# Kernel optimization log

Hardware: AMD Instinct MI355X
Metric: run time of the kernel (lower is better)

The kernel has to match this reference:

```python
import jax, jax.numpy as jnp
import numpy as np

N_NODES = 100000


def gcn_conv(x, edge_index, W, b):
    # PyG GCNConv: add self-loops, symmetric normalization D^-1/2 (A+I) D^-1/2,
    # linear transform then scatter-add aggregation at target nodes, plus bias.
    n = x.shape[0]
    loops = jnp.arange(n, dtype=edge_index.dtype)
    src = jnp.concatenate([edge_index[0], loops])
    dst = jnp.concatenate([edge_index[1], loops])
    deg = jax.ops.segment_sum(jnp.ones_like(dst, dtype=x.dtype), dst, num_segments=n)
    dinv = jnp.where(deg > 0, jax.lax.rsqrt(deg), 0.0)
    norm = dinv[src] * dinv[dst]  # [E+N]
    h = x @ W                      # transform first (small out dim)
    msg = h[src] * norm[:, None]   # per-edge gather + scale
    out = jax.ops.segment_sum(msg, dst, num_segments=n)
    return out + b


def setup_inputs() -> dict:
    key = jax.random.key(0)
    k1, k2, k3, k4 = jax.random.split(key, 4)
    N, E = N_NODES, 3200000
    x = jax.random.normal(k1, (N, 132), dtype=jnp.float32)
    edge_index = jax.random.randint(k2, (2, E), 0, N, dtype=jnp.int64)
    W1 = jax.random.normal(k3, (132, 16), dtype=jnp.float32) * 0.1
    b1 = jnp.zeros((16,), dtype=jnp.float32)
    W2 = jax.random.normal(k4, (16, 10), dtype=jnp.float32) * 0.25
    b2 = jnp.zeros((10,), dtype=jnp.float32)
    return {"x": x, "edge_index": edge_index, "W1": W1, "b1": b1, "W2": W2, "b2": b2}


def reference(x, edge_index, W1, b1, W2, b2):
    h = gcn_conv(x, edge_index, W1, b1)
    h = jax.nn.relu(h)
    # F.dropout(training=self.training) is identity in eval mode
    h = gcn_conv(h, edge_index, W2, b2)
    return jax.nn.log_softmax(h, axis=1)
```

## Files before the change

kernel.cpp:

```cpp
#include <hip/hip_runtime.h>
#include <math.h>


#define F_IN 132
#define F1   16
#define F2   10
#define BSH  7
#define BSPAN 128
#define NB   782
#define CAP  4608
#define SPB  12500
#define SPLIT_BLOCKS 256

__device__ __forceinline__ unsigned short f2bf(float f) {
    unsigned u = __float_as_uint(f);
    u += 0x7FFFu + ((u >> 16) & 1u);
    return (unsigned short)(u >> 16);
}
__device__ __forceinline__ float bflo(unsigned u) { return __uint_as_float(u << 16); }
__device__ __forceinline__ float bfhi(unsigned u) { return __uint_as_float(u & 0xFFFF0000u); }

__global__ __launch_bounds__(1024) void k_split(const int* __restrict__ src,
                                                const int* __restrict__ dst,
                                                int* __restrict__ gcur,
                                                unsigned* __restrict__ entries, int E) {
    __shared__ unsigned le[SPB];
    __shared__ int h0[1024];
    __shared__ int h1[1024];
    __shared__ int off[NB];
    const int t = threadIdx.x;
    const int lo = blockIdx.x * SPB;
    const int hi = min(E, lo + SPB);
    const int n4 = (hi - lo) >> 2;
    h0[t] = 0;
    __syncthreads();
    const int4* d4 = (const int4*)(dst + lo);
    const int4* s4 = (const int4*)(src + lo);
    for (int i = t; i < n4; i += 1024) {
        int4 d = d4[i];
        atomicAdd(&h0[d.x >> BSH], 1);
        atomicAdd(&h0[d.y >> BSH], 1);
        atomicAdd(&h0[d.z >> BSH], 1);
        atomicAdd(&h0[d.w >> BSH], 1);
    }
    __syncthreads();
    int c = h0[t];
    h1[t] = c;
    __syncthreads();
    for (int o = 1; o < 1024; o <<= 1) {
        int v = (t >= o) ? h1[t - o] : 0;
        __syncthreads();
        h1[t] += v;
        __syncthreads();
    }
    int excl = h1[t] - c;
    if (t < NB) {
        int g = t * CAP + (c ? atomicAdd(&gcur[t], c) : 0);
        off[t] = g - excl;
    }
    h0[t] = excl;
    __syncthreads();
    for (int i = t; i < n4; i += 1024) {
        int4 d = d4[i];
        int4 s = s4[i];
        int p;
        p = atomicAdd(&h0[d.x >> BSH], 1); le[p] = ((unsigned)(d.x & 127) << 17) | (unsigned)s.x;
        p = atomicAdd(&h0[d.y >> BSH], 1); le[p] = ((unsigned)(d.y & 127) << 17) | (unsigned)s.y;
        p = atomicAdd(&h0[d.z >> BSH], 1); le[p] = ((unsigned)(d.z & 127) << 17) | (unsigned)s.z;
        p = atomicAdd(&h0[d.w >> BSH], 1); le[p] = ((unsigned)(d.w & 127) << 17) | (unsigned)s.w;
    }
    __syncthreads();
    for (int bk = t; bk < NB; bk += 1024) {
        int s0 = bk ? h1[bk - 1] : 0;
        int e0 = h1[bk];
        unsigned* gp = entries + off[bk] + s0;
        for (int i = s0; i < e0; ++i) *gp++ = le[i];
    }
}

__global__ void k_sortB(const int* __restrict__ gcur, unsigned* __restrict__ entries,
                        int* __restrict__ rps, int* __restrict__ rpe,
                        float* __restrict__ dinv, int N) {
    __shared__ unsigned le[CAP];
    __shared__ int hist[BSPAN];
    __shared__ int scn[BSPAN];
    __shared__ int cur[BSPAN];
    const int b = blockIdx.x;
    const int t = threadIdx.x;
    const int cbase = b * CAP;
    const int cnt = gcur[b];
    if (t < BSPAN) hist[t] = 0;
    __syncthreads();
    for (int i = t; i < cnt; i += 256) {
        unsigned p = entries[cbase + i];
        le[i] = p;
        atomicAdd(&hist[p >> 17], 1);
    }
    __syncthreads();
    if (t < BSPAN) scn[t] = hist[t];
    __syncthreads();
    #pragma unroll
    for (int o = 1; o < BSPAN; o <<= 1) {
        int v = (t < BSPAN && t >= o) ? scn[t - o] : 0;
        __syncthreads();
        if (t < BSPAN) scn[t] += v;
        __syncthreads();
    }
    if (t < BSPAN) {
        const int node = b * BSPAN + t;
        const int begl = scn[t] - hist[t];
        cur[t] = cbase + begl;
        if (node < N) {
            rps[node] = cbase + begl;
            rpe[node] = cbase + begl + hist[t];
            dinv[node] = rsqrtf((float)hist[t] + 1.0f);
        }
    }
    __syncthreads();
    for (int i = t; i < cnt; i += 256) {
        unsigned p = le[i];
        int pos = atomicAdd(&cur[p >> 17], 1);
        entries[pos] = p & 0x1FFFFu;
    }
}

__global__ void k_xw1(const float* __restrict__ x, const float* __restrict__ W1,
                      const float* __restrict__ dinv, unsigned short* __restrict__ g1u, int N) {
    __shared__ float xs[16 * F_IN];
    __shared__ float wsm[F_IN * F1];
    const int t = threadIdx.x;
    const int base = blockIdx.x * 16;
    for (int idx = t; idx < 528; idx += 256)
        ((float4*)wsm)[idx] = ((const float4*)W1)[idx];
    int nrows = N - base; if (nrows > 16) nrows = 16;
    const float4* xp4 = (const float4*)(x + (size_t)base * F_IN);
    const int span4 = nrows * 33;
    for (int idx = t; idx < span4; idx += 256) ((float4*)xs)[idx] = xp4[idx];
    __syncthreads();
    const int r = t >> 4;
    const int c = t & 15;
    if (r < nrows) {
        float acc = 0.f;
        #pragma unroll 4
        for (int k = 0; k < F_IN; ++k) acc += xs[r * F_IN + k] * wsm[k * F1 + c];
        g1u[(size_t)(base + r) * 16 + c] = f2bf(acc * dinv[base + r]);
    }
}

#define ACCU8(q, B) \
    acc[(B)+0] += bflo((q).x); acc[(B)+1] += bfhi((q).x); \
    acc[(B)+2] += bflo((q).y); acc[(B)+3] += bfhi((q).y); \
    acc[(B)+4] += bflo((q).z); acc[(B)+5] += bfhi((q).z); \
    acc[(B)+6] += bflo((q).w); acc[(B)+7] += bfhi((q).w);

__global__ void k_agg1(const int* __restrict__ rps, const int* __restrict__ rpe,
                       const unsigned* __restrict__ ssrc, const unsigned short* __restrict__ g1u,
                       const float* __restrict__ dinv, const float* __restrict__ b1,
                       const float* __restrict__ W2, unsigned short* __restrict__ g2u, int N) {
    __shared__ float w2s[F1 * F2];
    __shared__ float b1s[F1];
    if (threadIdx.x < F1 * F2) w2s[threadIdx.x] = W2[threadIdx.x];
    if (threadIdx.x < F1) b1s[threadIdx.x] = b1[threadIdx.x];
    __syncthreads();
    const int d = blockIdx.x * blockDim.x + threadIdx.x;
    if (d >= N) return;
    const int beg = rps[d], end = rpe[d];
    float acc[F1];
    #pragma unroll
    for (int j = 0; j < F1; ++j) acc[j] = 0.f;
    int e = beg;
    for (; e + 1 < end; e += 2) {
        int s0 = (int)ssrc[e];
        int s1 = (int)ssrc[e + 1];
        const uint4* r0 = (const uint4*)(g1u + (size_t)s0 * 16);
        const uint4* r1 = (const uint4*)(g1u + (size_t)s1 * 16);
        uint4 a0 = r0[0], a1 = r0[1];
        uint4 c0 = r1[0], c1 = r1[1];
        ACCU8(a0, 0) ACCU8(a1, 8)
        ACCU8(c0, 0) ACCU8(c1, 8)
    }
    if (e < end) {
        int s = (int)ssrc[e];
        const uint4* r = (const uint4*)(g1u + (size_t)s * 16);
        uint4 a0 = r[0], a1 = r[1];
        ACCU8(a0, 0) ACCU8(a1, 8)
    }
    {
        const uint4* r = (const uint4*)(g1u + (size_t)d * 16);
        uint4 a0 = r[0], a1 = r[1];
        ACCU8(a0, 0) ACCU8(a1, 8)
    }
    const float dv = dinv[d];
    float tt[F1];
    #pragma unroll
    for (int j = 0; j < F1; ++j) {
        float v = dv * acc[j] + b1s[j];
        tt[j] = v > 0.f ? v : 0.f;
    }
    float o[F2];
    #pragma unroll
    for (int c = 0; c < F2; ++c) {
        float a = 0.f;
        #pragma unroll
        for (int j = 0; j < F1; ++j) a += tt[j] * w2s[j * F2 + c];
        o[c] = dv * a;
    }
    unsigned w0 = ((unsigned)f2bf(o[1]) << 16) | f2bf(o[0]);
    unsigned w1 = ((unsigned)f2bf(o[3]) << 16) | f2bf(o[2]);
    unsigned w2 = ((unsigned)f2bf(o[5]) << 16) | f2bf(o[4]);
    unsigned w3 = ((unsigned)f2bf(o[7]) << 16) | f2bf(o[6]);
    unsigned w4 = ((unsigned)f2bf(o[9]) << 16) | f2bf(o[8]);
    uint4* op = (uint4*)(g2u + (size_t)d * 16);
    op[0] = make_uint4(w0, w1, w2, w3);
    op[1] = make_uint4(w4, 0u, 0u, 0u);
}

__global__ void k_agg2(const int* __restrict__ rps, const int* __restrict__ rpe,
                       const unsigned* __restrict__ ssrc, const unsigned short* __restrict__ g2u,
                       const float* __restrict__ dinv, const float* __restrict__ b2,
                       float* __restrict__ out, int N) {
    __shared__ float b2s[F2];
    if (threadIdx.x < F2) b2s[threadIdx.x] = b2[threadIdx.x];
    __syncthreads();
    const int d = blockIdx.x * blockDim.x + threadIdx.x;
    if (d >= N) return;
    const int beg = rps[d], end = rpe[d];
    float acc[F2];
    #pragma unroll
    for (int c = 0; c < F2; ++c) acc[c] = 0.f;
    int e = beg;
    for (; e + 1 < end; e += 2) {
        int s0 = (int)ssrc[e];
        int s1 = (int)ssrc[e + 1];
        const unsigned short* p0 = g2u + (size_t)s0 * 16;
        const unsigned short* p1 = g2u + (size_t)s1 * 16;
        uint4 a0 = *(const uint4*)(p0);
        unsigned a4 = *(const unsigned*)(p0 + 8);
        uint4 c0 = *(const uint4*)(p1);
        unsigned c4 = *(const unsigned*)(p1 + 8);
        ACCU8(a0, 0)
        acc[8] += bflo(a4); acc[9] += bfhi(a4);
        ACCU8(c0, 0)
        acc[8] += bflo(c4); acc[9] += bfhi(c4);
    }
    if (e < end) {
        int s = (int)ssrc[e];
        const unsigned short* p = g2u + (size_t)s * 16;
        uint4 a0 = *(const uint4*)(p);
        unsigned a4 = *(const unsigned*)(p + 8);
        ACCU8(a0, 0)
        acc[8] += bflo(a4); acc[9] += bfhi(a4);
    }
    {
        const unsigned short* p = g2u + (size_t)d * 16;
        uint4 a0 = *(const uint4*)(p);
        unsigned a4 = *(const unsigned*)(p + 8);
        ACCU8(a0, 0)
        acc[8] += bflo(a4); acc[9] += bfhi(a4);
    }
    const float dv = dinv[d];
    float v[F2];
    float m = -INFINITY;
    #pragma unroll
    for (int c = 0; c < F2; ++c) {
        v[c] = dv * acc[c] + b2s[c];
        m = fmaxf(m, v[c]);
    }
    float ssum = 0.f;
    #pragma unroll
    for (int c = 0; c < F2; ++c) ssum += expf(v[c] - m);
    float ls = logf(ssum);
    float* op = out + (size_t)d * F2;
    #pragma unroll
    for (int c = 0; c < F2; ++c) op[c] = v[c] - m - ls;
}

extern "C" void kernel_launch(void* const* d_in, const int* in_sizes, int n_in,
                              void* d_out, int out_size, void* d_ws, size_t ws_size,
                              hipStream_t stream) {
    const float* x  = (const float*)d_in[0];
    const int*   ei = (const int*)  d_in[1];
    const float* W1 = (const float*)d_in[2];
    const float* b1 = (const float*)d_in[3];
    const float* W2 = (const float*)d_in[4];
    const float* b2 = (const float*)d_in[5];
    float* out = (float*)d_out;

    const int N = in_sizes[0] / F_IN;
    const int E = in_sizes[1] / 2;
    const int* src = ei;
    const int* dst = ei + E;

    char* w = (char*)d_ws;
    int*            gcur    = (int*)w;            w += ((size_t)NB * 4 + 255) & ~255ull;
    int*            rps     = (int*)w;            w += ((size_t)N * 4 + 255) & ~255ull;
    int*            rpe     = (int*)w;            w += ((size_t)N * 4 + 255) & ~255ull;
    float*          dinv    = (float*)w;          w += ((size_t)N * 4 + 255) & ~255ull;
    unsigned short* g1u     = (unsigned short*)w; w += ((size_t)N * 16 * 2 + 255) & ~255ull;
    unsigned short* g2u     = (unsigned short*)w; w += ((size_t)N * 16 * 2 + 255) & ~255ull;
    unsigned*       entries = (unsigned*)w;

    hipMemsetAsync(gcur, 0, (size_t)NB * 4, stream);
    k_split<<<SPLIT_BLOCKS, 1024, 0, stream>>>(src, dst, gcur, entries, E);
    k_sortB<<<NB, 256, 0, stream>>>(gcur, entries, rps, rpe, dinv, N);
    k_xw1  <<<(N + 15) / 16, 256, 0, stream>>>(x, W1, dinv, g1u, N);
    k_agg1 <<<(N + 255) / 256, 256, 0, stream>>>(rps, rpe, entries, g1u, dinv, b1, W2, g2u, N);
    k_agg2 <<<(N + 255) / 256, 256, 0, stream>>>(rps, rpe, entries, g2u, dinv, b2, out, N);
}
```

Measured before the change: 169.3 us.

## Split each node's edge aggregation across four lanes with shuffle reduction

Both aggregation kernels now assign four threads per destination node, each walking a strided quarter of the node's edge list, then combine partial sums with xor shuffles before lane 0 finishes the epilogue. This raises parallelism and memory-level concurrency for the gather-heavy loops, since about 32 edges per node were previously serialized in one thread. The output write in the second layer is vectorized as well. It costs four times the threads and shuffle overhead, and three of every four lanes sit idle during the epilogue.

```diff
diff --git a/kernel.cpp b/kernel.cpp
--- a/kernel.cpp
+++ b/kernel.cpp
@@ -147,11 +147,11 @@
     }
 }
 
-#define ACCU8(q, B) \
-    acc[(B)+0] += bflo((q).x); acc[(B)+1] += bfhi((q).x); \
-    acc[(B)+2] += bflo((q).y); acc[(B)+3] += bfhi((q).y); \
-    acc[(B)+4] += bflo((q).z); acc[(B)+5] += bfhi((q).z); \
-    acc[(B)+6] += bflo((q).w); acc[(B)+7] += bfhi((q).w);
+#define ACCU8(qv, B) \
+    acc[(B)+0] += bflo((qv).x); acc[(B)+1] += bfhi((qv).x); \
+    acc[(B)+2] += bflo((qv).y); acc[(B)+3] += bfhi((qv).y); \
+    acc[(B)+4] += bflo((qv).z); acc[(B)+5] += bfhi((qv).z); \
+    acc[(B)+6] += bflo((qv).w); acc[(B)+7] += bfhi((qv).w);
 
 __global__ void k_agg1(const int* __restrict__ rps, const int* __restrict__ rpe,
                        const unsigned* __restrict__ ssrc, const unsigned short* __restrict__ g1u,
@@ -162,57 +162,54 @@
     if (threadIdx.x < F1 * F2) w2s[threadIdx.x] = W2[threadIdx.x];
     if (threadIdx.x < F1) b1s[threadIdx.x] = b1[threadIdx.x];
     __syncthreads();
-    const int d = blockIdx.x * blockDim.x + threadIdx.x;
+    const int gid = blockIdx.x * blockDim.x + threadIdx.x;
+    const int d = gid >> 2;
+    const int q = gid & 3;
     if (d >= N) return;
     const int beg = rps[d], end = rpe[d];
     float acc[F1];
     #pragma unroll
     for (int j = 0; j < F1; ++j) acc[j] = 0.f;
-    int e = beg;
-    for (; e + 1 < end; e += 2) {
-        int s0 = (int)ssrc[e];
-        int s1 = (int)ssrc[e + 1];
-        const uint4* r0 = (const uint4*)(g1u + (size_t)s0 * 16);
-        const uint4* r1 = (const uint4*)(g1u + (size_t)s1 * 16);
-        uint4 a0 = r0[0], a1 = r0[1];
-        uint4 c0 = r1[0], c1 = r1[1];
-        ACCU8(a0, 0) ACCU8(a1, 8)
-        ACCU8(c0, 0) ACCU8(c1, 8)
-    }
-    if (e < end) {
+    for (int e = beg + q; e < end; e += 4) {
         int s = (int)ssrc[e];
         const uint4* r = (const uint4*)(g1u + (size_t)s * 16);
         uint4 a0 = r[0], a1 = r[1];
         ACCU8(a0, 0) ACCU8(a1, 8)
     }
-    {
+    if (q == 0) {
         const uint4* r = (const uint4*)(g1u + (size_t)d * 16);
         uint4 a0 = r[0], a1 = r[1];
         ACCU8(a0, 0) ACCU8(a1, 8)
     }
-    const float dv = dinv[d];
-    float tt[F1];
-    #pragma unroll
-    for (int j = 0; j < F1; ++j) {
-        float v = dv * acc[j] + b1s[j];
-        tt[j] = v > 0.f ? v : 0.f;
-    }
-    float o[F2];
-    #pragma unroll
-    for (int c = 0; c < F2; ++c) {
-        float a = 0.f;
+    #pragma unroll
+    for (int j = 0; j < F1; ++j) acc[j] += __shfl_xor(acc[j], 1);
+    #pragma unroll
+    for (int j = 0; j < F1; ++j) acc[j] += __shfl_xor(acc[j], 2);
+    if (q == 0) {
+        const float dv = dinv[d];
+        float tt[F1];
         #pragma unroll
-        for (int j = 0; j < F1; ++j) a += tt[j] * w2s[j * F2 + c];
-        o[c] = dv * a;
-    }
-    unsigned w0 = ((unsigned)f2bf(o[1]) << 16) | f2bf(o[0]);
-    unsigned w1 = ((unsigned)f2bf(o[3]) << 16) | f2bf(o[2]);
-    unsigned w2 = ((unsigned)f2bf(o[5]) << 16) | f2bf(o[4]);
-    unsigned w3 = ((unsigned)f2bf(o[7]) << 16) | f2bf(o[6]);
-    unsigned w4 = ((unsigned)f2bf(o[9]) << 16) | f2bf(o[8]);
-    uint4* op = (uint4*)(g2u + (size_t)d * 16);
-    op[0] = make_uint4(w0, w1, w2, w3);
-    op[1] = make_uint4(w4, 0u, 0u, 0u);
+        for (int j = 0; j < F1; ++j) {
+            float v = dv * acc[j] + b1s[j];
+            tt[j] = v > 0.f ? v : 0.f;
+        }
+        float o[F2];
+        #pragma unroll
+        for (int c = 0; c < F2; ++c) {
+            float a = 0.f;
+            #pragma unroll
+            for (int j = 0; j < F1; ++j) a += tt[j] * w2s[j * F2 + c];
+            o[c] = dv * a;
+        }
+        unsigned w0 = ((unsigned)f2bf(o[1]) << 16) | f2bf(o[0]);
+        unsigned w1 = ((unsigned)f2bf(o[3]) << 16) | f2bf(o[2]);
+        unsigned w2 = ((unsigned)f2bf(o[5]) << 16) | f2bf(o[4]);
+        unsigned w3 = ((unsigned)f2bf(o[7]) << 16) | f2bf(o[6]);
+        unsigned w4 = ((unsigned)f2bf(o[9]) << 16) | f2bf(o[8]);
+        uint4* op = (uint4*)(g2u + (size_t)d * 16);
+        op[0] = make_uint4(w0, w1, w2, w3);
+        op[1] = make_uint4(w4, 0u, 0u, 0u);
+    }
 }
 
 __global__ void k_agg2(const int* __restrict__ rps, const int* __restrict__ rpe,
@@ -222,28 +219,15 @@
     __shared__ float b2s[F2];
     if (threadIdx.x < F2) b2s[threadIdx.x] = b2[threadIdx.x];
     __syncthreads();
-    const int d = blockIdx.x * blockDim.x + threadIdx.x;
+    const int gid = blockIdx.x * blockDim.x + threadIdx.x;
+    const int d = gid >> 2;
+    const int q = gid & 3;
     if (d >= N) return;
     const int beg = rps[d], end = rpe[d];
     float acc[F2];
     #pragma unroll
     for (int c = 0; c < F2; ++c) acc[c] = 0.f;
-    int e = beg;
-    for (; e + 1 < end; e += 2) {
-        int s0 = (int)ssrc[e];
-        int s1 = (int)ssrc[e + 1];
-        const unsigned short* p0 = g2u + (size_t)s0 * 16;
-        const unsigned short* p1 = g2u + (size_t)s1 * 16;
-        uint4 a0 = *(const uint4*)(p0);
-        unsigned a4 = *(const unsigned*)(p0 + 8);
-        uint4 c0 = *(const uint4*)(p1);
-        unsigned c4 = *(const unsigned*)(p1 + 8);
-        ACCU8(a0, 0)
-        acc[8] += bflo(a4); acc[9] += bfhi(a4);
-        ACCU8(c0, 0)
-        acc[8] += bflo(c4); acc[9] += bfhi(c4);
-    }
-    if (e < end) {
+    for (int e = beg + q; e < end; e += 4) {
         int s = (int)ssrc[e];
         const unsigned short* p = g2u + (size_t)s * 16;
         uint4 a0 = *(const uint4*)(p);
@@ -251,28 +235,35 @@
         ACCU8(a0, 0)
         acc[8] += bflo(a4); acc[9] += bfhi(a4);
     }
-    {
+    if (q == 0) {
         const unsigned short* p = g2u + (size_t)d * 16;
         uint4 a0 = *(const uint4*)(p);
         unsigned a4 = *(const unsigned*)(p + 8);
         ACCU8(a0, 0)
         acc[8] += bflo(a4); acc[9] += bfhi(a4);
     }
-    const float dv = dinv[d];
-    float v[F2];
-    float m = -INFINITY;
-    #pragma unroll
-    for (int c = 0; c < F2; ++c) {
-        v[c] = dv * acc[c] + b2s[c];
-        m = fmaxf(m, v[c]);
-    }
-    float ssum = 0.f;
-    #pragma unroll
-    for (int c = 0; c < F2; ++c) ssum += expf(v[c] - m);
-    float ls = logf(ssum);
-    float* op = out + (size_t)d * F2;
-    #pragma unroll
-    for (int c = 0; c < F2; ++c) op[c] = v[c] - m - ls;
+    #pragma unroll
+    for (int c = 0; c < F2; ++c) acc[c] += __shfl_xor(acc[c], 1);
+    #pragma unroll
+    for (int c = 0; c < F2; ++c) acc[c] += __shfl_xor(acc[c], 2);
+    if (q == 0) {
+        const float dv = dinv[d];
+        float v[F2];
+        float m = -INFINITY;
+        #pragma unroll
+        for (int c = 0; c < F2; ++c) {
+            v[c] = dv * acc[c] + b2s[c];
+            m = fmaxf(m, v[c]);
+        }
+        float ssum = 0.f;
+        #pragma unroll
+        for (int c = 0; c < F2; ++c) ssum += expf(v[c] - m);
+        float ls = logf(ssum);
+        float* op = out + (size_t)d * F2;
+        *(float4*)(op)     = make_float4(v[0]-m-ls, v[1]-m-ls, v[2]-m-ls, v[3]-m-ls);
+        *(float4*)(op + 4) = make_float4(v[4]-m-ls, v[5]-m-ls, v[6]-m-ls, v[7]-m-ls);
+        *(float2*)(op + 8) = make_float2(v[8]-m-ls, v[9]-m-ls);
+    }
 }
 
 extern "C" void kernel_launch(void* const* d_in, const int* in_sizes, int n_in,
@@ -304,6 +295,6 @@
     k_split<<<SPLIT_BLOCKS, 1024, 0, stream>>>(src, dst, gcur, entries, E);
     k_sortB<<<NB, 256, 0, stream>>>(gcur, entries, rps, rpe, dinv, N);
     k_xw1  <<<(N + 15) / 16, 256, 0, stream>>>(x, W1, dinv, g1u, N);
-    k_agg1 <<<(N + 255) / 256, 256, 0, stream>>>(rps, rpe, entries, g1u, dinv, b1, W2, g2u, N);
-    k_agg2 <<<(N + 255) / 256, 256, 0, stream>>>(rps, rpe, entries, g2u, dinv, b2, out, N);
-}
+    k_agg1 <<<(4 * N + 255) / 256, 256, 0, stream>>>(rps, rpe, entries, g1u, dinv, b1, W2, g2u, N);
+    k_agg2 <<<(4 * N + 255) / 256, 256, 0, stream>>>(rps, rpe, entries, g2u, dinv, b2, out, N);
+}
```

Result: faster. 148.2 us (-12.5%).
